# Kernel tuning notes

Measured on AMD Instinct MI355X. Metric: run time of the kernel, lower is better.

## Reference

```python
import jax, jax.numpy as jnp
import numpy as np

# SRU config from the module: 3 layers, highway_bias=0, rescale=True, no layer_norm.
# rescale factor from sru package: sqrt(1 + exp(highway_bias)*2)
SCALE_X = (1.0 + np.exp(0.0) * 2.0) ** 0.5

IMG_DIM, T, HID, NCLS, B = 512, 12, 1024, 51, 2048


def _sru_layer(x, W, vc, b):
    # x: (T, B, d_in); W: (d_in, k*d); vc: (2, d) gate-recurrence vectors; b: (2, d) biases
    Tn, Bn, d_in = x.shape
    d = vc.shape[1]
    k = W.shape[1] // d  # 4 if d_in != d else 3
    U = jnp.einsum('tbi,ij->tbj', x, W).reshape(Tn, Bn, k, d)
    u0, u1, u2 = U[:, :, 0], U[:, :, 1], U[:, :, 2]
    resid = U[:, :, 3] if k == 4 else x  # projected residual when dims differ
    vf, vr = vc[0], vc[1]
    bf, br = b[0], b[1]

    def step(c, inp):
        u0t, u1t, u2t, xt = inp
        f = jax.nn.sigmoid(u1t + vf * c + bf)          # forget gate (uses c_{t-1})
        c_new = f * c + (1.0 - f) * u0t                # cell update
        r = jax.nn.sigmoid(u2t + vr * c_new + br)      # reset gate (uses c_t, as in SRU CUDA)
        h = r * jnp.tanh(c_new) + (1.0 - r) * xt * SCALE_X  # highway with rescale
        return c_new, h

    c0 = jnp.zeros((Bn, d), x.dtype)
    c_last, h = jax.lax.scan(step, c0, (u0, u1, u2, resid))
    return h, c_last


def setup_inputs() -> dict:
    key = jax.random.key(0)
    ks = jax.random.split(key, 12)
    inp = {}
    inp['x'] = jax.random.normal(ks[0], (B, T, IMG_DIM), jnp.float32)
    # layer 0: 512 -> 1024, k=4; layers 1,2: 1024 -> 1024, k=3
    inp['W0'] = jax.random.normal(ks[1], (IMG_DIM, 4 * HID), jnp.float32) / np.sqrt(IMG_DIM)
    inp['W1'] = jax.random.normal(ks[2], (HID, 3 * HID), jnp.float32) / np.sqrt(HID)
    inp['W2'] = jax.random.normal(ks[3], (HID, 3 * HID), jnp.float32) / np.sqrt(HID)
    inp['vc0'] = jax.random.normal(ks[4], (2, HID), jnp.float32) * 0.1
    inp['vc1'] = jax.random.normal(ks[5], (2, HID), jnp.float32) * 0.1
    inp['vc2'] = jax.random.normal(ks[6], (2, HID), jnp.float32) * 0.1
    inp['b0'] = jnp.zeros((2, HID), jnp.float32)
    inp['b1'] = jnp.zeros((2, HID), jnp.float32)
    inp['b2'] = jnp.zeros((2, HID), jnp.float32)
    inp['fc_w'] = jax.random.normal(ks[7], (HID, NCLS), jnp.float32) / np.sqrt(HID)
    inp['fc_b'] = jnp.zeros((NCLS,), jnp.float32)
    return inp


def reference(x, W0, W1, W2, vc0, vc1, vc2, b0, b1, b2, fc_w, fc_b):
    h = jnp.transpose(x, (1, 0, 2))  # (T, B, img_dim)
    for W, vc, b in ((W0, vc0, b0), (W1, vc1, b1), (W2, vc2, b2)):
        h, _ = _sru_layer(h, W, vc, b)
    # dropout layers are identity in eval mode
    logits = jnp.einsum('tbh,hc->tbc', h, fc_w) + fc_b  # (T, B, num_class)
    return jnp.mean(logits, axis=0)  # (B, num_class)
```

## Files before the change

### kernel.cpp

```cpp
#include <hip/hip_runtime.h>
#include <math.h>

#define TSTEPS 12
#define BATCH  2048
#define IMG    512
#define HIDN   1024
#define NCLASS 51
#define SCALE_X 1.7320508075688772f

typedef __attribute__((ext_vector_type(8))) _Float16 f16x8;
typedef __attribute__((ext_vector_type(2))) _Float16 f16x2;
typedef __attribute__((ext_vector_type(4))) float    f32x4;

__device__ __forceinline__ float sigf(float x) {
    return 1.f / (1.f + __expf(-x));
}

template<int NCOMP>
__global__ __launch_bounds__(256)
void gemm_sru(const _Float16* __restrict__ A, const _Float16* __restrict__ Bt,
              const _Float16* __restrict__ resid,
              const float* __restrict__ vc, const float* __restrict__ bias,
              _Float16* __restrict__ hout, float* __restrict__ hbar, int K) {
    constexpr int BM = 192, BN = 32 * NCOMP, HBN = BN / 2, NJ = NCOMP;
    constexpr int S_A = 2 * BM * 32;
    constexpr int S_B = 2 * BN * 32;
    constexpr int EPAD = BN + 8;
    constexpr int EPI = BM * EPAD;
    constexpr int TOT = (S_A + S_B) > EPI ? (S_A + S_B) : EPI;
    __shared__ _Float16 smem[TOT];

    const int tid  = threadIdx.x;
    const int lane = tid & 63;
    const int w    = tid >> 6;
    const int bm   = blockIdx.y * BM;
    const int bn   = blockIdx.x * BN;

    const bool isA  = (w < 2);
    const _Float16* splane = isA ? A : Bt;
    const int srow0 = isA ? (bm + (w & 1) * 96) : (bn + (w & 1) * HBN);
    const int nrows = isA ? 96 : HBN;
    const int lrow  = lane >> 2;
    const int lcol  = (lane & 3) * 8;

    const int wy = (w >> 1) * 96;
    const int wx = (w & 1) * HBN;

    f32x4 acc[6][NJ];
    #pragma unroll
    for (int i = 0; i < 6; ++i)
        #pragma unroll
        for (int j = 0; j < NJ; ++j) acc[i][j] = (f32x4){0.f, 0.f, 0.f, 0.f};

    const int kq = (lane >> 4) * 8;
    const int mr = lane & 15;

    const _Float16* gbase = splane + (size_t)(srow0 + lrow) * K + lcol;

    auto stage = [&](int buf, int k0) {
        const _Float16* g = gbase + k0;
        _Float16* l = isA ? (smem + buf * BM * 32 + (w & 1) * (96 * 32))
                          : (smem + S_A + buf * BN * 32 + (w & 1) * (HBN * 32));
        for (int j = 0; j < nrows / 16; ++j)
            __builtin_amdgcn_global_load_lds(
                (const __attribute__((address_space(1))) unsigned int*)(g + (size_t)j * 16 * K),
                (__attribute__((address_space(3))) unsigned int*)(l + j * 512),
                16, 0, 0);
    };

    stage(0, 0);

    int cur = 0;
    for (int k0 = 0; k0 < K; k0 += 32) {
        __syncthreads();
        if (k0 + 32 < K) stage(cur ^ 1, k0 + 32);

        const _Float16* la = smem + cur * BM * 32;
        const _Float16* lb = smem + S_A + cur * BN * 32;
        f16x8 a[6], b[NJ];
        #pragma unroll
        for (int i = 0; i < 6; ++i)
            a[i] = *(const f16x8*)&la[(wy + i * 16 + mr) * 32 + kq];
        #pragma unroll
        for (int j = 0; j < NJ; ++j)
            b[j] = *(const f16x8*)&lb[(wx + j * 16 + mr) * 32 + kq];
        #pragma unroll
        for (int i = 0; i < 6; ++i)
            #pragma unroll
            for (int j = 0; j < NJ; ++j)
                acc[i][j] = __builtin_amdgcn_mfma_f32_16x16x32_f16(a[i], b[j], acc[i][j], 0, 0, 0);
        cur ^= 1;
    }

    __syncthreads();
    {
        _Float16 (*uld)[EPAD] = (_Float16 (*)[EPAD])smem;
        const int r0 = (lane >> 4) << 2;
        #pragma unroll
        for (int i = 0; i < 6; ++i)
            #pragma unroll
            for (int j = 0; j < NJ; ++j)
                #pragma unroll
                for (int r = 0; r < 4; ++r)
                    uld[wy + i * 16 + r0 + r][wx + j * 16 + mr] =
                        (_Float16)acc[i][j][r];
    }
    __syncthreads();

    {
        _Float16 (*uld)[EPAD] = (_Float16 (*)[EPAD])smem;
        const int bl   = tid >> 4;
        const int ch0  = (tid & 15) * 2;
        const int gcol = blockIdx.x * 32 + ch0;
        const int gb   = bm / 12 + bl;

        const float2 vf  = *(const float2*)&vc[gcol];
        const float2 vr  = *(const float2*)&vc[HIDN + gcol];
        const float2 bfv = *(const float2*)&bias[gcol];
        const float2 brv = *(const float2*)&bias[HIDN + gcol];

        float c0 = 0.f, c1 = 0.f, s0 = 0.f, s1 = 0.f;
        #pragma unroll
        for (int t = 0; t < TSTEPS; ++t) {
            const int row = bl * 12 + t;
            const float u0a = (float)uld[row][(ch0    ) * NCOMP + 0];
            const float u1a = (float)uld[row][(ch0    ) * NCOMP + 1];
            const float u2a = (float)uld[row][(ch0    ) * NCOMP + 2];
            const float u0b = (float)uld[row][(ch0 + 1) * NCOMP + 0];
            const float u1b = (float)uld[row][(ch0 + 1) * NCOMP + 1];
            const float u2b = (float)uld[row][(ch0 + 1) * NCOMP + 2];
            float xta, xtb;
            if (NCOMP == 4) {
                xta = (float)uld[row][(ch0    ) * 4 + 3];
                xtb = (float)uld[row][(ch0 + 1) * 4 + 3];
            } else {
                const f16x2 xv = *(const f16x2*)&resid[(size_t)(bm + row) * HIDN + gcol];
                xta = (float)xv[0]; xtb = (float)xv[1];
            }

            const float f0 = sigf(u1a + vf.x * c0 + bfv.x);
            c0 = f0 * c0 + (1.f - f0) * u0a;
            const float r0_ = sigf(u2a + vr.x * c0 + brv.x);
            const float th0 = 2.f * sigf(2.f * c0) - 1.f;
            const float hv0 = r0_ * th0 + (1.f - r0_) * xta * SCALE_X;

            const float f1 = sigf(u1b + vf.y * c1 + bfv.y);
            c1 = f1 * c1 + (1.f - f1) * u0b;
            const float r1_ = sigf(u2b + vr.y * c1 + brv.y);
            const float th1 = 2.f * sigf(2.f * c1) - 1.f;
            const float hv1 = r1_ * th1 + (1.f - r1_) * xtb * SCALE_X;

            if (hout) {
                f16x2 hv = { (_Float16)hv0, (_Float16)hv1 };
                *(f16x2*)&hout[(size_t)(bm + row) * HIDN + gcol] = hv;
            }
            s0 += hv0; s1 += hv1;
        }
        if (hbar) {
            float2 hb = make_float2(s0 * (1.f / TSTEPS), s1 * (1.f / TSTEPS));
            *(float2*)&hbar[(size_t)gb * HIDN + gcol] = hb;
        }
    }
}

__global__ __launch_bounds__(256)
void wsplit_t(const float* __restrict__ W, _Float16* __restrict__ Wt,
              int K, int N, int ncomp) {
    __shared__ float tile[32][33];
    const int bn = blockIdx.x * 32;
    const int bk = blockIdx.y * 32;
    const int tx = threadIdx.x & 31;
    const int ty = threadIdx.x >> 5;
    #pragma unroll
    for (int i = 0; i < 32; i += 8)
        tile[ty + i][tx] = W[(size_t)(bk + ty + i) * N + bn + tx];
    __syncthreads();
    #pragma unroll
    for (int i = 0; i < 32; i += 8) {
        const int n = bn + ty + i;
        const int nr = (n & 1023) * ncomp + (n >> 10);
        Wt[(size_t)nr * K + bk + tx] = (_Float16)tile[tx][ty + i];
    }
}

__global__ __launch_bounds__(256)
void esplit(const float* __restrict__ src, _Float16* __restrict__ dst, int n) {
    int i = blockIdx.x * 256 + threadIdx.x;
    if (i < n) dst[i] = (_Float16)src[i];
}

__global__ __launch_bounds__(64)
void final_fc(const float* __restrict__ hbar, const float* __restrict__ fcw,
              const float* __restrict__ fcb, float* __restrict__ out) {
    __shared__ float hrow[HIDN];
    const int b = blockIdx.x;
    for (int i = threadIdx.x; i < HIDN; i += 64)
        hrow[i] = hbar[(size_t)b * HIDN + i];
    __syncthreads();

    const int c = threadIdx.x;
    if (c < NCLASS) {
        float acc = fcb[c];
        #pragma unroll 8
        for (int k = 0; k < HIDN; ++k)
            acc = fmaf(hrow[k], fcw[(size_t)k * NCLASS + c], acc);
        out[(size_t)b * NCLASS + c] = acc;
    }
}

extern "C" void kernel_launch(void* const* d_in, const int* in_sizes, int n_in,
                              void* d_out, int out_size, void* d_ws, size_t ws_size,
                              hipStream_t stream) {
    const float* x   = (const float*)d_in[0];
    const float* W0  = (const float*)d_in[1];
    const float* W1  = (const float*)d_in[2];
    const float* W2  = (const float*)d_in[3];
    const float* vc0 = (const float*)d_in[4];
    const float* vc1 = (const float*)d_in[5];
    const float* vc2 = (const float*)d_in[6];
    const float* b0  = (const float*)d_in[7];
    const float* b1  = (const float*)d_in[8];
    const float* b2  = (const float*)d_in[9];
    const float* fcw = (const float*)d_in[10];
    const float* fcb = (const float*)d_in[11];
    float* out = (float*)d_out;

    char* ws = (char*)d_ws;
    size_t off = 0;
    auto carve = [&](size_t bytes) { char* p = ws + off; off = (off + bytes + 255) & ~255ull; return p; };

    _Float16* W0t = (_Float16*)carve((size_t)4096 * 512 * 2);
    _Float16* W1t = (_Float16*)carve((size_t)3072 * 1024 * 2);
    _Float16* W2t = (_Float16*)carve((size_t)3072 * 1024 * 2);
    const size_t W_BYTES = off;

    const size_t PER_B = 12ull * 512 * 2 + 2ull * 12 * 1024 * 2 + 1024ull * 4 + 1024;
    int CB = 32;
    if      (W_BYTES + 2048ull * PER_B <= ws_size) CB = 2048;
    else if (W_BYTES + 1024ull * PER_B <= ws_size) CB = 1024;
    else if (W_BYTES +  512ull * PER_B <= ws_size) CB = 512;
    else if (W_BYTES +  256ull * PER_B <= ws_size) CB = 256;
    else if (W_BYTES +  128ull * PER_B <= ws_size) CB = 128;
    else if (W_BYTES +   64ull * PER_B <= ws_size) CB = 64;
    const int MC = CB * TSTEPS;

    _Float16* x16  = (_Float16*)carve((size_t)MC * 512 * 2);
    _Float16* hA16 = (_Float16*)carve((size_t)MC * 1024 * 2);
    _Float16* hB16 = (_Float16*)carve((size_t)MC * 1024 * 2);
    float*    hbar = (float*)carve((size_t)CB * 1024 * 4);

    const dim3 blk256(256);

    wsplit_t<<<dim3(4096 / 32, 512 / 32),  blk256, 0, stream>>>(W0, W0t, 512, 4096, 4);
    wsplit_t<<<dim3(3072 / 32, 1024 / 32), blk256, 0, stream>>>(W1, W1t, 1024, 3072, 3);
    wsplit_t<<<dim3(3072 / 32, 1024 / 32), blk256, 0, stream>>>(W2, W2t, 1024, 3072, 3);

    for (int cb = 0; cb < BATCH / CB; ++cb) {
        const float* xc   = x   + (size_t)cb * CB * TSTEPS * IMG;
        float*       outc = out + (size_t)cb * CB * NCLASS;

        esplit<<<dim3((MC * 512) / 256), blk256, 0, stream>>>(xc, x16, MC * 512);
        gemm_sru<4><<<dim3(4096 / 128, MC / 192), blk256, 0, stream>>>(
            x16, W0t, nullptr, vc0, b0, hA16, nullptr, 512);

        gemm_sru<3><<<dim3(3072 / 96, MC / 192), blk256, 0, stream>>>(
            hA16, W1t, hA16, vc1, b1, hB16, nullptr, 1024);

        gemm_sru<3><<<dim3(3072 / 96, MC / 192), blk256, 0, stream>>>(
            hB16, W2t, hB16, vc2, b2, nullptr, hbar, 1024);

        final_fc<<<dim3(CB), dim3(64), 0, stream>>>(hbar, fcw, fcb, outc);
    }
}
```

Baseline: 853.5 us.

## Use 32x32 MFMA tiles, widen k=3 layer tiles, split epilogue into two passes

After: 1.091 ms. 1.28x slower.

```diff
diff --git a/kernel.cpp b/kernel.cpp
--- a/kernel.cpp
+++ b/kernel.cpp
@@ -8,27 +8,28 @@
 #define NCLASS 51
 #define SCALE_X 1.7320508075688772f
 
-typedef __attribute__((ext_vector_type(8))) _Float16 f16x8;
-typedef __attribute__((ext_vector_type(2))) _Float16 f16x2;
-typedef __attribute__((ext_vector_type(4))) float    f32x4;
+typedef __attribute__((ext_vector_type(8)))  _Float16 f16x8;
+typedef __attribute__((ext_vector_type(2)))  _Float16 f16x2;
+typedef __attribute__((ext_vector_type(16))) float    f32x16;
 
 __device__ __forceinline__ float sigf(float x) {
     return 1.f / (1.f + __expf(-x));
 }
 
-template<int NCOMP>
+template<int TJ, int NCOMP>
 __global__ __launch_bounds__(256)
 void gemm_sru(const _Float16* __restrict__ A, const _Float16* __restrict__ Bt,
               const _Float16* __restrict__ resid,
               const float* __restrict__ vc, const float* __restrict__ bias,
               _Float16* __restrict__ hout, float* __restrict__ hbar, int K) {
-    constexpr int BM = 192, BN = 32 * NCOMP, HBN = BN / 2, NJ = NCOMP;
+    constexpr int BM = 192, BN = 64 * TJ, HBN = BN / 2;
+    constexpr int NCH = BN / NCOMP;
     constexpr int S_A = 2 * BM * 32;
     constexpr int S_B = 2 * BN * 32;
     constexpr int EPAD = BN + 8;
-    constexpr int EPI = BM * EPAD;
+    constexpr int EPI = 96 * EPAD;
     constexpr int TOT = (S_A + S_B) > EPI ? (S_A + S_B) : EPI;
-    __shared__ _Float16 smem[TOT];
+    __shared__ __align__(16) _Float16 smem[TOT];
 
     const int tid  = threadIdx.x;
     const int lane = tid & 63;
@@ -46,14 +47,16 @@
     const int wy = (w >> 1) * 96;
     const int wx = (w & 1) * HBN;
 
-    f32x4 acc[6][NJ];
+    f32x16 acc[3][TJ];
     #pragma unroll
-    for (int i = 0; i < 6; ++i)
+    for (int i = 0; i < 3; ++i)
         #pragma unroll
-        for (int j = 0; j < NJ; ++j) acc[i][j] = (f32x4){0.f, 0.f, 0.f, 0.f};
-
-    const int kq = (lane >> 4) * 8;
-    const int mr = lane & 15;
+        for (int j = 0; j < TJ; ++j)
+            #pragma unroll
+            for (int r = 0; r < 16; ++r) acc[i][j][r] = 0.f;
+
+    const int l5  = lane >> 5;
+    const int m32 = lane & 31;
 
     const _Float16* gbase = splane + (size_t)(srow0 + lrow) * K + lcol;
 
@@ -77,91 +80,115 @@
 
         const _Float16* la = smem + cur * BM * 32;
         const _Float16* lb = smem + S_A + cur * BN * 32;
-        f16x8 a[6], b[NJ];
         #pragma unroll
-        for (int i = 0; i < 6; ++i)
-            a[i] = *(const f16x8*)&la[(wy + i * 16 + mr) * 32 + kq];
-        #pragma unroll
-        for (int j = 0; j < NJ; ++j)
-            b[j] = *(const f16x8*)&lb[(wx + j * 16 + mr) * 32 + kq];
-        #pragma unroll
-        for (int i = 0; i < 6; ++i)
-            #pragma unroll
-            for (int j = 0; j < NJ; ++j)
-                acc[i][j] = __builtin_amdgcn_mfma_f32_16x16x32_f16(a[i], b[j], acc[i][j], 0, 0, 0);
+        for (int ks = 0; ks < 2; ++ks) {
+            const int ko = ks * 16 + l5 * 8;
+            f16x8 a[3], b[TJ];
+            #pragma unroll
+            for (int i = 0; i < 3; ++i)
+                a[i] = *(const f16x8*)&la[(wy + i * 32 + m32) * 32 + ko];
+            #pragma unroll
+            for (int j = 0; j < TJ; ++j)
+                b[j] = *(const f16x8*)&lb[(wx + j * 32 + m32) * 32 + ko];
+            #pragma unroll
+            for (int i = 0; i < 3; ++i)
+                #pragma unroll
+                for (int j = 0; j < TJ; ++j)
+                    acc[i][j] = __builtin_amdgcn_mfma_f32_32x32x16_f16(
+                        a[i], b[j], acc[i][j], 0, 0, 0);
+        }
         cur ^= 1;
     }
 
-    __syncthreads();
-    {
-        _Float16 (*uld)[EPAD] = (_Float16 (*)[EPAD])smem;
-        const int r0 = (lane >> 4) << 2;
-        #pragma unroll
-        for (int i = 0; i < 6; ++i)
-            #pragma unroll
-            for (int j = 0; j < NJ; ++j)
+    _Float16 (*uld)[EPAD] = (_Float16 (*)[EPAD])smem;
+    const int bl  = tid >> 5;
+    const int pr  = tid & 31;
+    #pragma unroll
+    for (int pass = 0; pass < 2; ++pass) {
+        __syncthreads();
+        if ((w >> 1) == pass) {
+            #pragma unroll
+            for (int i = 0; i < 3; ++i)
                 #pragma unroll
-                for (int r = 0; r < 4; ++r)
-                    uld[wy + i * 16 + r0 + r][wx + j * 16 + mr] =
-                        (_Float16)acc[i][j][r];
-    }
-    __syncthreads();
-
-    {
-        _Float16 (*uld)[EPAD] = (_Float16 (*)[EPAD])smem;
-        const int bl   = tid >> 4;
-        const int ch0  = (tid & 15) * 2;
-        const int gcol = blockIdx.x * 32 + ch0;
-        const int gb   = bm / 12 + bl;
-
-        const float2 vf  = *(const float2*)&vc[gcol];
-        const float2 vr  = *(const float2*)&vc[HIDN + gcol];
-        const float2 bfv = *(const float2*)&bias[gcol];
-        const float2 brv = *(const float2*)&bias[HIDN + gcol];
-
-        float c0 = 0.f, c1 = 0.f, s0 = 0.f, s1 = 0.f;
-        #pragma unroll
-        for (int t = 0; t < TSTEPS; ++t) {
-            const int row = bl * 12 + t;
-            const float u0a = (float)uld[row][(ch0    ) * NCOMP + 0];
-            const float u1a = (float)uld[row][(ch0    ) * NCOMP + 1];
-            const float u2a = (float)uld[row][(ch0    ) * NCOMP + 2];
-            const float u0b = (float)uld[row][(ch0 + 1) * NCOMP + 0];
-            const float u1b = (float)uld[row][(ch0 + 1) * NCOMP + 1];
-            const float u2b = (float)uld[row][(ch0 + 1) * NCOMP + 2];
-            float xta, xtb;
-            if (NCOMP == 4) {
-                xta = (float)uld[row][(ch0    ) * 4 + 3];
-                xtb = (float)uld[row][(ch0 + 1) * 4 + 3];
-            } else {
-                const f16x2 xv = *(const f16x2*)&resid[(size_t)(bm + row) * HIDN + gcol];
-                xta = (float)xv[0]; xtb = (float)xv[1];
+                for (int j = 0; j < TJ; ++j)
+                    #pragma unroll
+                    for (int r = 0; r < 16; ++r) {
+                        const int row = i * 32 + (r & 3) + 8 * (r >> 2) + 4 * l5;
+                        uld[row][wx + j * 32 + m32] = (_Float16)acc[i][j][r];
+                    }
+        }
+        __syncthreads();
+
+        const int prm = pr & (NCH / 2 - 1);
+        const int rep = (NCH == 64) ? 1 : 2;
+        for (int q = 0; q < rep; ++q) {
+            const int blq  = bl + q * 8;
+            const int blx  = (rep == 1) ? bl : (tid >> 4);
+            if (rep == 2 && q == 1) break;
+            const int bloc = (rep == 1) ? blq : (blx & 7);
+            const int extra= (rep == 1) ? 0 : (blx >> 3);
+            (void)extra; (void)bloc;
+            const int b8   = (rep == 1) ? bl : (blx & 7);
+            if (rep == 2 && (blx >> 3) != 0 && false) {}
+            const int bln  = b8;
+            const int ch0  = ((rep == 1) ? pr : (tid & 15) * 1) * 2;
+            const int ch   = (rep == 1) ? ch0 : (prm * 2);
+            (void)ch0;
+            const int gcol = blockIdx.x * NCH + ((rep == 1) ? pr * 2 : prm * 2);
+            const int gb   = bm / 12 + pass * 8 + bln;
+
+            const float2 vf  = *(const float2*)&vc[gcol];
+            const float2 vr  = *(const float2*)&vc[HIDN + gcol];
+            const float2 bfv = *(const float2*)&bias[gcol];
+            const float2 brv = *(const float2*)&bias[HIDN + gcol];
+
+            float c0 = 0.f, c1 = 0.f, s0 = 0.f, s1 = 0.f;
+            const int chp = (rep == 1) ? pr * 2 : prm * 2;
+            #pragma unroll
+            for (int t = 0; t < TSTEPS; ++t) {
+                const int row = bln * 12 + t;
+                const float u0a = (float)uld[row][(chp    ) * NCOMP + 0];
+                const float u1a = (float)uld[row][(chp    ) * NCOMP + 1];
+                const float u2a = (float)uld[row][(chp    ) * NCOMP + 2];
+                const float u0b = (float)uld[row][(chp + 1) * NCOMP + 0];
+                const float u1b = (float)uld[row][(chp + 1) * NCOMP + 1];
+                const float u2b = (float)uld[row][(chp + 1) * NCOMP + 2];
+                float xta, xtb;
+                if (NCOMP == 4) {
+                    xta = (float)uld[row][(chp    ) * 4 + 3];
+                    xtb = (float)uld[row][(chp + 1) * 4 + 3];
+                } else {
+                    const f16x2 xv = *(const f16x2*)
+                        &resid[(size_t)(bm + pass * 96 + row) * HIDN + gcol];
+                    xta = (float)xv[0]; xtb = (float)xv[1];
+                }
+
+                const float f0 = sigf(u1a + vf.x * c0 + bfv.x);
+                c0 = f0 * c0 + (1.f - f0) * u0a;
+                const float r0_ = sigf(u2a + vr.x * c0 + brv.x);
+                const float th0 = 2.f * sigf(2.f * c0) - 1.f;
+                const float hv0 = r0_ * th0 + (1.f - r0_) * xta * SCALE_X;
+
+                const float f1 = sigf(u1b + vf.y * c1 + bfv.y);
+                c1 = f1 * c1 + (1.f - f1) * u0b;
+                const float r1_ = sigf(u2b + vr.y * c1 + brv.y);
+                const float th1 = 2.f * sigf(2.f * c1) - 1.f;
+                const float hv1 = r1_ * th1 + (1.f - r1_) * xtb * SCALE_X;
+
+                if (hout && (rep == 1 || bl < 8)) {
+                    f16x2 hv = { (_Float16)hv0, (_Float16)hv1 };
+                    *(f16x2*)&hout[(size_t)(bm + pass * 96 + row) * HIDN + gcol] = hv;
+                }
+                s0 += hv0; s1 += hv1;
             }
-
-            const float f0 = sigf(u1a + vf.x * c0 + bfv.x);
-            c0 = f0 * c0 + (1.f - f0) * u0a;
-            const float r0_ = sigf(u2a + vr.x * c0 + brv.x);
-            const float th0 = 2.f * sigf(2.f * c0) - 1.f;
-            const float hv0 = r0_ * th0 + (1.f - r0_) * xta * SCALE_X;
-
-            const float f1 = sigf(u1b + vf.y * c1 + bfv.y);
-            c1 = f1 * c1 + (1.f - f1) * u0b;
-            const float r1_ = sigf(u2b + vr.y * c1 + brv.y);
-            const float th1 = 2.f * sigf(2.f * c1) - 1.f;
-            const float hv1 = r1_ * th1 + (1.f - r1_) * xtb * SCALE_X;
-
-            if (hout) {
-                f16x2 hv = { (_Float16)hv0, (_Float16)hv1 };
-                *(f16x2*)&hout[(size_t)(bm + row) * HIDN + gcol] = hv;
+            if (hbar && (rep == 1 || bl < 8)) {
+                float2 hb = make_float2(s0 * (1.f / TSTEPS), s1 * (1.f / TSTEPS));
+                *(float2*)&hbar[(size_t)gb * HIDN + gcol] = hb;
             }
-            s0 += hv0; s1 += hv1;
         }
-        if (hbar) {
-            float2 hb = make_float2(s0 * (1.f / TSTEPS), s1 * (1.f / TSTEPS));
-            *(float2*)&hbar[(size_t)gb * HIDN + gcol] = hb;
-        }
-    }
-}
+    }
+}
+
 
 __global__ __launch_bounds__(256)
 void wsplit_t(const float* __restrict__ W, _Float16* __restrict__ Wt,
@@ -260,13 +287,13 @@
         float*       outc = out + (size_t)cb * CB * NCLASS;
 
         esplit<<<dim3((MC * 512) / 256), blk256, 0, stream>>>(xc, x16, MC * 512);
-        gemm_sru<4><<<dim3(4096 / 128, MC / 192), blk256, 0, stream>>>(
+        gemm_sru<2, 4><<<dim3(4096 / 128, MC / 192), blk256, 0, stream>>>(
             x16, W0t, nullptr, vc0, b0, hA16, nullptr, 512);
 
-        gemm_sru<3><<<dim3(3072 / 96, MC / 192), blk256, 0, stream>>>(
+        gemm_sru<3, 3><<<dim3(3072 / 192, MC / 192), blk256, 0, stream>>>(
             hA16, W1t, hA16, vc1, b1, hB16, nullptr, 1024);
 
-        gemm_sru<3><<<dim3(3072 / 96, MC / 192), blk256, 0, stream>>>(
+        gemm_sru<3, 3><<<dim3(3072 / 192, MC / 192), blk256, 0, stream>>>(
             hB16, W2t, hB16, vc2, b2, nullptr, hbar, 1024);
 
         final_fc<<<dim3(CB), dim3(64), 0, stream>>>(hbar, fcw, fcb, outc);
```
